# Kernel tuning notes

Hardware: AMD Instinct MI355X
Metric: run time of the kernel (lower is better)

Reference implementation:

```python
import jax, jax.numpy as jnp
import numpy as np

N = 100_000   # nodes
E = 1_600_000 # edges
F = 128       # node feature dim
H = 128       # hidden dim
A = 8         # num actions


def setup_inputs() -> dict:
    key = jax.random.key(0)
    ks = jax.random.split(key, 8)
    x = jax.random.normal(ks[0], (N, F), dtype=jnp.float32)
    edge_index = jax.random.randint(ks[1], (2, E), 0, N, dtype=jnp.int64)
    s1 = 1.0 / np.sqrt(F)
    s2 = 1.0 / np.sqrt(H)
    W1 = jax.random.uniform(ks[2], (F, H), jnp.float32, -s1, s1)
    b1 = jnp.zeros((H,), jnp.float32)
    W2 = jax.random.uniform(ks[3], (H, H), jnp.float32, -s2, s2)
    b2 = jnp.zeros((H,), jnp.float32)
    Wfc = jax.random.uniform(ks[4], (H, A), jnp.float32, -s2, s2)
    bfc = jax.random.uniform(ks[5], (A,), jnp.float32, -s2, s2)
    return {"x": x, "edge_index": edge_index, "W1": W1, "b1": b1,
            "W2": W2, "b2": b2, "Wfc": Wfc, "bfc": bfc}


def _gcn_norm(edge_index):
    # PyG GCNConv default: add self-loops, symmetric deg^{-1/2} A deg^{-1/2}
    src, dst = edge_index[0], edge_index[1]
    loop = jnp.arange(N, dtype=src.dtype)
    src_f = jnp.concatenate([src, loop])
    dst_f = jnp.concatenate([dst, loop])
    deg = jax.ops.segment_sum(jnp.ones((E + N,), jnp.float32), dst_f,
                              num_segments=N)
    dis = jax.lax.rsqrt(deg)  # deg >= 1 thanks to self-loops
    norm = dis[src_f] * dis[dst_f]  # [E+N]
    return src_f, dst_f, norm


def _gcn_conv(h, W, b, src_f, dst_f, norm):
    hw = h @ W                              # [N, out]
    msg = hw[src_f] * norm[:, None]         # gather + scale: [E+N, out]
    out = jax.ops.segment_sum(msg, dst_f, num_segments=N)  # scatter-add
    return out + b


def reference(x, edge_index, W1, b1, W2, b2, Wfc, bfc):
    src_f, dst_f, norm = _gcn_norm(edge_index)
    h = jax.nn.relu(_gcn_conv(x, W1, b1, src_f, dst_f, norm))
    h = jax.nn.relu(_gcn_conv(h, W2, b2, src_f, dst_f, norm))
    return h @ Wfc + bfc  # [N, A] per-node Q-values
```

## Files before the change

kernel.cpp:

```cpp
#include <hip/hip_runtime.h>
#include <hip/hip_bf16.h>

#define NN 100000
#define EE 1600000
#define FF 128
#define HH 128
#define AA 8

#define NBIN 782
#define CAP  3072

typedef unsigned int u32;
typedef unsigned short ushort_t;

using bf16x8 = __attribute__((ext_vector_type(8))) short;
using f32x4  = __attribute__((ext_vector_type(4))) float;

__device__ inline u32 packbf2(float a, float b) {
    __hip_bfloat162 t;
    t.x = __float2bfloat16(a);
    t.y = __float2bfloat16(b);
    return *(u32*)&t;
}
__device__ inline float2 unpackbf2(u32 v) {
    union { u32 u; float f; } lo, hi;
    lo.u = v << 16;
    hi.u = v & 0xffff0000u;
    return make_float2(lo.f, hi.f);
}

__global__ void k_init(int* bincnt) {
    int i = blockIdx.x * blockDim.x + threadIdx.x;
    if (i < NBIN) bincnt[i] = 0;
}

__global__ __launch_bounds__(256)
void k_wt(const float* __restrict__ W, u32* __restrict__ WT) {
    __shared__ float tile[32][33];
    const int tk = (blockIdx.x >> 2) * 32;
    const int tn = (blockIdx.x & 3) * 32;
    const int t = threadIdx.x;
    {
        int r = t >> 3, c4 = t & 7;
        float4 v = *(const float4*)&W[(tk + r) * 128 + tn + c4 * 4];
        tile[r][c4 * 4 + 0] = v.x;
        tile[r][c4 * 4 + 1] = v.y;
        tile[r][c4 * 4 + 2] = v.z;
        tile[r][c4 * 4 + 3] = v.w;
    }
    __syncthreads();
    {
        int nl = t >> 3, w = t & 7;
        u32 w0 = packbf2(tile[w * 4 + 0][nl], tile[w * 4 + 1][nl]);
        u32 w1 = packbf2(tile[w * 4 + 2][nl], tile[w * 4 + 3][nl]);
        *(uint2*)&WT[(size_t)(tn + nl) * 64 + (tk >> 1) + w * 2] = make_uint2(w0, w1);
    }
}

__global__ __launch_bounds__(256)
void k_bin(const int* __restrict__ ei, int* __restrict__ g_bincnt,
           int2* __restrict__ binbuf, int e) {
    __shared__ int cnt_l[NBIN];
    __shared__ int base_l[NBIN];
    __shared__ int cur_l[NBIN];
    const int t = threadIdx.x;
    for (int q = t; q < NBIN; q += 256) cnt_l[q] = 0;
    __syncthreads();
    const int per = (e + gridDim.x - 1) / gridDim.x;
    const int i0 = blockIdx.x * per;
    const int i1 = min(e, i0 + per);
    for (int i = i0 + t; i < i1; i += 256) {
        int dst = ei[e + i];
        atomicAdd(&cnt_l[dst >> 7], 1);
    }
    __syncthreads();
    for (int q = t; q < NBIN; q += 256) {
        base_l[q] = cnt_l[q] ? atomicAdd(&g_bincnt[q], cnt_l[q]) : 0;
        cur_l[q] = 0;
    }
    __syncthreads();
    for (int i = i0 + t; i < i1; i += 256) {
        int dst = ei[e + i];
        int src = ei[i];
        int p = dst >> 7;
        int pos = base_l[p] + atomicAdd(&cur_l[p], 1);
        if (pos < CAP)
            binbuf[(size_t)p * CAP + pos] = make_int2(src, dst);
    }
}

__global__ __launch_bounds__(1024)
void k_binscan(const int* __restrict__ bincnt, int* __restrict__ binbase) {
    __shared__ int s[1024];
    const int t = threadIdx.x;
    int v = (t < NBIN) ? min(bincnt[t], CAP) : 0;
    s[t] = v;
    __syncthreads();
    for (int off = 1; off < 1024; off <<= 1) {
        int x = (t >= off) ? s[t - off] : 0;
        __syncthreads();
        s[t] += x;
        __syncthreads();
    }
    if (t < NBIN) binbase[t] = s[t] - v;
}

__global__ __launch_bounds__(256)
void k_csr(const int2* __restrict__ binbuf, const int* __restrict__ g_bincnt,
           const int* __restrict__ binbase, int* __restrict__ row_start,
           float* __restrict__ dis, int* __restrict__ csr_src, int n)
{
    __shared__ int deg[128], s[128], cur[128];
    const int p = blockIdx.x;
    const int t = threadIdx.x;
    const int plo = p << 7;
    if (t < 128) { deg[t] = 0; cur[t] = 0; }
    __syncthreads();
    const int c = min(g_bincnt[p], CAP);
    const int2* slab = &binbuf[(size_t)p * CAP];
    for (int i = t; i < c; i += 256)
        atomicAdd(&deg[slab[i].y - plo], 1);
    __syncthreads();
    if (t < 128) s[t] = deg[t];
    __syncthreads();
    for (int off = 1; off < 128; off <<= 1) {
        int x = (t < 128 && t >= off) ? s[t - off] : 0;
        __syncthreads();
        if (t < 128) s[t] += x;
        __syncthreads();
    }
    const int base = binbase[p];
    if (t < 128) {
        int node = plo + t;
        if (node <= n) row_start[node] = base + s[t] - deg[t];
        if (node < n)  dis[node] = rsqrtf((float)deg[t] + 1.0f);
        if (p == NBIN - 1 && t == 127) row_start[n] = base + s[127];
    }
    __syncthreads();
    for (int i = t; i < c; i += 256) {
        int2 sd = slab[i];
        int nl = sd.y - plo;
        int pos = base + (s[nl] - deg[nl]) + atomicAdd(&cur[nl], 1);
        csr_src[pos] = sd.x;
    }
}

#define LDK 136

template<int AF32>
__global__ __launch_bounds__(256)
void k_gemm_mfma(const void* __restrict__ Ain, const u32* __restrict__ WT,
                 const float* __restrict__ dis, u32* __restrict__ outbf, int n)
{
    __shared__ ushort_t sA[64 * LDK];
    __shared__ ushort_t sB[128 * LDK];
    const int tid = threadIdx.x;
    const int row0 = blockIdx.x * 64;

    if (AF32) {
        const float* A = (const float*)Ain;
#pragma unroll
        for (int i = 0; i < 8; i++) {
            int f = tid + i * 256;
            int r = f >> 5, c4 = f & 31;
            int gr = row0 + r; if (gr >= n) gr = n - 1;
            float4 v = *(const float4*)&A[(size_t)gr * 128 + c4 * 4];
            *(uint2*)&sA[r * LDK + c4 * 4] =
                make_uint2(packbf2(v.x, v.y), packbf2(v.z, v.w));
        }
    } else {
        const u32* A = (const u32*)Ain;
#pragma unroll
        for (int i = 0; i < 4; i++) {
            int f = tid + i * 256;
            int r = f >> 4, q = f & 15;
            int gr = row0 + r; if (gr >= n) gr = n - 1;
            uint4 v = *(const uint4*)&A[(size_t)gr * 64 + q * 4];
            *(uint4*)&sA[r * LDK + q * 8] = v;
        }
    }
#pragma unroll
    for (int i = 0; i < 8; i++) {
        int f = tid + i * 256;
        int r = f >> 4, q = f & 15;
        uint4 v = *(const uint4*)&WT[(size_t)r * 64 + q * 4];
        *(uint4*)&sB[r * LDK + q * 8] = v;
    }
    __syncthreads();

    const int l   = tid & 63;
    const int w   = tid >> 6;
    const int col = l & 15;
    const int g   = l >> 4;
    const ushort_t* pa = &sA[(w * 16 + col) * LDK + g * 8];
    const ushort_t* pb = &sB[col * LDK + g * 8];

    f32x4 acc[8] = {};
#pragma unroll
    for (int ks = 0; ks < 4; ks++) {
        bf16x8 a = *(const bf16x8*)(pa + ks * 32);
#pragma unroll
        for (int cf = 0; cf < 8; cf++) {
            bf16x8 b = *(const bf16x8*)(pb + (size_t)cf * 16 * LDK + ks * 32);
            acc[cf] = __builtin_amdgcn_mfma_f32_16x16x32_bf16(a, b, acc[cf], 0, 0, 0);
        }
    }

    const int grow0 = row0 + w * 16 + g * 4;
    float dvr[4];
#pragma unroll
    for (int r = 0; r < 4; r++)
        dvr[r] = (grow0 + r < n) ? dis[grow0 + r] : 0.f;
#pragma unroll
    for (int cf = 0; cf < 8; cf++) {
#pragma unroll
        for (int r = 0; r < 4; r++) {
            float val = acc[cf][r] * dvr[r];
            float oth = __shfl_xor(val, 1);
            if (!(l & 1) && (grow0 + r < n))
                outbf[(size_t)(grow0 + r) * 64 + (cf * 16 + col) / 2] = packbf2(val, oth);
        }
    }
}

__launch_bounds__(256)
__global__ void k_agg(const int* __restrict__ csr_src,
                      const int* __restrict__ row_start,
                      const u32* __restrict__ hw,
                      const float* __restrict__ dis,
                      const float* __restrict__ b,
                      u32* __restrict__ out, int n)
{
    int node = blockIdx.x * 4 + (threadIdx.x >> 6);
    if (node >= n) return;
    int lane = threadIdx.x & 63;
    int beg = row_start[node];
    int end = row_start[node + 1];

    float2 acc = unpackbf2(hw[(long long)node * 64 + lane]);
    int i = beg;
    for (; i + 15 < end; i += 16) {
        int idx[16];
#pragma unroll
        for (int u = 0; u < 16; u++) idx[u] = csr_src[i + u];
        u32 a[16];
#pragma unroll
        for (int u = 0; u < 16; u++) a[u] = hw[(long long)idx[u] * 64 + lane];
        float sx = 0.f, sy = 0.f;
#pragma unroll
        for (int u = 0; u < 16; u++) {
            float2 v = unpackbf2(a[u]);
            sx += v.x; sy += v.y;
        }
        acc.x += sx; acc.y += sy;
    }
    if (i + 7 < end) {
        int idx[8];
#pragma unroll
        for (int u = 0; u < 8; u++) idx[u] = csr_src[i + u];
        u32 a[8];
#pragma unroll
        for (int u = 0; u < 8; u++) a[u] = hw[(long long)idx[u] * 64 + lane];
        float sx = 0.f, sy = 0.f;
#pragma unroll
        for (int u = 0; u < 8; u++) {
            float2 v = unpackbf2(a[u]);
            sx += v.x; sy += v.y;
        }
        acc.x += sx; acc.y += sy;
        i += 8;
    }
    for (; i + 1 < end; i += 2) {
        int s0 = csr_src[i];
        int s1 = csr_src[i + 1];
        float2 v0 = unpackbf2(hw[(long long)s0 * 64 + lane]);
        float2 v1 = unpackbf2(hw[(long long)s1 * 64 + lane]);
        acc.x += v0.x + v1.x;
        acc.y += v0.y + v1.y;
    }
    if (i < end) {
        float2 v0 = unpackbf2(hw[(long long)csr_src[i] * 64 + lane]);
        acc.x += v0.x;
        acc.y += v0.y;
    }
    float d = dis[node];
    float2 bb = *(const float2*)&b[lane * 2];
    float ox = fmaxf(fmaf(d, acc.x, bb.x), 0.f);
    float oy = fmaxf(fmaf(d, acc.y, bb.y), 0.f);
    out[(long long)node * 64 + lane] = packbf2(ox, oy);
}

__launch_bounds__(256)
__global__ void k_fc(const u32* __restrict__ hbf,
                     const float* __restrict__ Wfc,
                     const float* __restrict__ bfc,
                     float* __restrict__ out, int n)
{
    __shared__ float sW[128 * 8];
    __shared__ float sH[32][132];
    const int tid = threadIdx.x;
    *(float4*)&sW[tid * 4] = *(const float4*)&Wfc[tid * 4];
    const int n0 = blockIdx.x * 32;
#pragma unroll
    for (int i = 0; i < 4; i++) {
        int f = tid + i * 256;
        int node = f >> 5;
        int wq = f & 31;
        int gn = n0 + node; if (gn >= n) gn = n - 1;
        uint2 v = *(const uint2*)&hbf[(long long)gn * 64 + wq * 2];
        float2 p0 = unpackbf2(v.x);
        float2 p1 = unpackbf2(v.y);
        sH[node][wq * 4 + 0] = p0.x;
        sH[node][wq * 4 + 1] = p0.y;
        sH[node][wq * 4 + 2] = p1.x;
        sH[node][wq * 4 + 3] = p1.y;
    }
    __syncthreads();
    const int node = tid >> 3;
    const int a = tid & 7;
    float acc = bfc[a];
#pragma unroll
    for (int k = 0; k < 128; k++)
        acc += sH[node][k] * sW[k * 8 + a];
    int gn = n0 + node;
    if (gn < n) out[gn * 8 + a] = acc;
}

extern "C" void kernel_launch(void* const* d_in, const int* in_sizes, int n_in,
                              void* d_out, int out_size, void* d_ws, size_t ws_size,
                              hipStream_t stream) {
    const float* x   = (const float*)d_in[0];
    const int*   ei  = (const int*)d_in[1];
    const float* W1  = (const float*)d_in[2];
    const float* b1  = (const float*)d_in[3];
    const float* W2  = (const float*)d_in[4];
    const float* b2  = (const float*)d_in[5];
    const float* Wfc = (const float*)d_in[6];
    const float* bfc = (const float*)d_in[7];
    float* out = (float*)d_out;

    const int n = NN, e = EE;

    char* ws = (char*)d_ws;
    const size_t MB = 1 << 20;
    float* dis       = (float*)(ws);
    int*   row_start = (int*)  (ws + 512 * 1024);
    int*   bincnt    = (int*)  (ws + 1 * MB);
    int*   binbase   = (int*)  (ws + 1 * MB + 8192);
    u32*   WT1       = (u32*)  (ws + 1 * MB + 65536);
    u32*   WT2       = (u32*)  (ws + 1 * MB + 2 * 65536);
    int2*  binbuf    = (int2*) (ws + 2 * MB);
    int*   csr_src   = (int*)  (ws + 22 * MB);
    u32*   hwbf      = (u32*)  (ws + 29 * MB);
    u32*   hbf       = (u32*)  (ws + 55 * MB);

    k_init<<<(NBIN + 255) / 256, 256, 0, stream>>>(bincnt);
    k_wt<<<16, 256, 0, stream>>>(W1, WT1);
    k_wt<<<16, 256, 0, stream>>>(W2, WT2);

    k_bin<<<128, 256, 0, stream>>>(ei, bincnt, binbuf, e);
    k_binscan<<<1, 1024, 0, stream>>>(bincnt, binbase);
    k_csr<<<NBIN, 256, 0, stream>>>(binbuf, bincnt, binbase, row_start, dis, csr_src, n);

    const int gemm_grid = (n + 63) / 64;
    const int agg_grid  = (n + 3) / 4;

    k_gemm_mfma<1><<<gemm_grid, 256, 0, stream>>>(x, WT1, dis, hwbf, n);
    k_agg<<<agg_grid, 256, 0, stream>>>(csr_src, row_start, hwbf, dis, b1, hbf, n);

    k_gemm_mfma<0><<<gemm_grid, 256, 0, stream>>>(hbf, WT2, dis, hwbf, n);
    k_agg<<<agg_grid, 256, 0, stream>>>(csr_src, row_start, hwbf, dis, b2, hbf, n);

    k_fc<<<(n + 31) / 32, 256, 0, stream>>>(hbf, Wfc, bfc, out, n);
}
```

Before: 247.5 us.

## Vectorize edge binning loads and split wave halves across edges in aggregation

The binning kernel now runs 256 blocks of 1024 threads, and each thread reads int4 groups of edge indices, which cuts load instruction count and spreads the work over more CUs. The aggregation kernel has each half-wave take alternate edges, with every lane loading 8 bytes (4 bf16 features) instead of 4. The two halves are then combined with a cross-half shuffle before the bias, ReLU and store. This doubles the gathers in flight per wave and widens each memory access, at the cost of the shuffle reduction and half the lanes idling in the epilogue.

```diff
diff --git a/kernel.cpp b/kernel.cpp
--- a/kernel.cpp
+++ b/kernel.cpp
@@ -9,6 +9,7 @@
 
 #define NBIN 782
 #define CAP  3072
+#define BINBLK 256
 
 typedef unsigned int u32;
 typedef unsigned short ushort_t;
@@ -57,35 +58,53 @@
     }
 }
 
-__global__ __launch_bounds__(256)
+__global__ __launch_bounds__(1024)
 void k_bin(const int* __restrict__ ei, int* __restrict__ g_bincnt,
            int2* __restrict__ binbuf, int e) {
     __shared__ int cnt_l[NBIN];
     __shared__ int base_l[NBIN];
     __shared__ int cur_l[NBIN];
     const int t = threadIdx.x;
-    for (int q = t; q < NBIN; q += 256) cnt_l[q] = 0;
-    __syncthreads();
-    const int per = (e + gridDim.x - 1) / gridDim.x;
+    for (int q = t; q < NBIN; q += 1024) cnt_l[q] = 0;
+    __syncthreads();
+    const int per = (((e + BINBLK - 1) / BINBLK) + 3) & ~3;
     const int i0 = blockIdx.x * per;
     const int i1 = min(e, i0 + per);
-    for (int i = i0 + t; i < i1; i += 256) {
-        int dst = ei[e + i];
-        atomicAdd(&cnt_l[dst >> 7], 1);
-    }
-    __syncthreads();
-    for (int q = t; q < NBIN; q += 256) {
+    int i = i0 + t * 4;
+    for (; i + 3 < i1; i += 4096) {
+        int4 d4 = *(const int4*)&ei[e + i];
+        atomicAdd(&cnt_l[d4.x >> 7], 1);
+        atomicAdd(&cnt_l[d4.y >> 7], 1);
+        atomicAdd(&cnt_l[d4.z >> 7], 1);
+        atomicAdd(&cnt_l[d4.w >> 7], 1);
+    }
+    for (int j = i; j < min(i + 4, i1); j++)
+        atomicAdd(&cnt_l[ei[e + j] >> 7], 1);
+    __syncthreads();
+    for (int q = t; q < NBIN; q += 1024) {
         base_l[q] = cnt_l[q] ? atomicAdd(&g_bincnt[q], cnt_l[q]) : 0;
         cur_l[q] = 0;
     }
     __syncthreads();
-    for (int i = i0 + t; i < i1; i += 256) {
-        int dst = ei[e + i];
-        int src = ei[i];
+    i = i0 + t * 4;
+    for (; i + 3 < i1; i += 4096) {
+        int4 s4 = *(const int4*)&ei[i];
+        int4 d4 = *(const int4*)&ei[e + i];
+        int p0 = d4.x >> 7, p1 = d4.y >> 7, p2 = d4.z >> 7, p3 = d4.w >> 7;
+        int q0 = base_l[p0] + atomicAdd(&cur_l[p0], 1);
+        int q1 = base_l[p1] + atomicAdd(&cur_l[p1], 1);
+        int q2 = base_l[p2] + atomicAdd(&cur_l[p2], 1);
+        int q3 = base_l[p3] + atomicAdd(&cur_l[p3], 1);
+        if (q0 < CAP) binbuf[(size_t)p0 * CAP + q0] = make_int2(s4.x, d4.x);
+        if (q1 < CAP) binbuf[(size_t)p1 * CAP + q1] = make_int2(s4.y, d4.y);
+        if (q2 < CAP) binbuf[(size_t)p2 * CAP + q2] = make_int2(s4.z, d4.z);
+        if (q3 < CAP) binbuf[(size_t)p3 * CAP + q3] = make_int2(s4.w, d4.w);
+    }
+    for (int j = i; j < min(i + 4, i1); j++) {
+        int dst = ei[e + j], src = ei[j];
         int p = dst >> 7;
         int pos = base_l[p] + atomicAdd(&cur_l[p], 1);
-        if (pos < CAP)
-            binbuf[(size_t)p * CAP + pos] = make_int2(src, dst);
+        if (pos < CAP) binbuf[(size_t)p * CAP + pos] = make_int2(src, dst);
     }
 }
 
@@ -233,61 +252,58 @@
 {
     int node = blockIdx.x * 4 + (threadIdx.x >> 6);
     if (node >= n) return;
-    int lane = threadIdx.x & 63;
-    int beg = row_start[node];
-    int end = row_start[node + 1];
-
-    float2 acc = unpackbf2(hw[(long long)node * 64 + lane]);
+    const int lane = threadIdx.x & 63;
+    const int half = lane >> 5;
+    const int sl   = lane & 31;
+    const int beg = row_start[node];
+    const int end = row_start[node + 1];
+
+    float4 acc = make_float4(0.f, 0.f, 0.f, 0.f);
+    if (!half) {
+        uint2 s = *(const uint2*)&hw[(size_t)node * 64 + sl * 2];
+        float2 a = unpackbf2(s.x), c = unpackbf2(s.y);
+        acc = make_float4(a.x, a.y, c.x, c.y);
+    }
     int i = beg;
     for (; i + 15 < end; i += 16) {
-        int idx[16];
-#pragma unroll
-        for (int u = 0; u < 16; u++) idx[u] = csr_src[i + u];
-        u32 a[16];
-#pragma unroll
-        for (int u = 0; u < 16; u++) a[u] = hw[(long long)idx[u] * 64 + lane];
-        float sx = 0.f, sy = 0.f;
-#pragma unroll
-        for (int u = 0; u < 16; u++) {
-            float2 v = unpackbf2(a[u]);
-            sx += v.x; sy += v.y;
-        }
-        acc.x += sx; acc.y += sy;
-    }
-    if (i + 7 < end) {
         int idx[8];
 #pragma unroll
-        for (int u = 0; u < 8; u++) idx[u] = csr_src[i + u];
-        u32 a[8];
-#pragma unroll
-        for (int u = 0; u < 8; u++) a[u] = hw[(long long)idx[u] * 64 + lane];
-        float sx = 0.f, sy = 0.f;
+        for (int u = 0; u < 8; u++) idx[u] = csr_src[i + 2 * u + half];
+        uint2 v[8];
+#pragma unroll
+        for (int u = 0; u < 8; u++) v[u] = *(const uint2*)&hw[(size_t)idx[u] * 64 + sl * 2];
 #pragma unroll
         for (int u = 0; u < 8; u++) {
-            float2 v = unpackbf2(a[u]);
-            sx += v.x; sy += v.y;
-        }
-        acc.x += sx; acc.y += sy;
-        i += 8;
+            float2 a = unpackbf2(v[u].x), c = unpackbf2(v[u].y);
+            acc.x += a.x; acc.y += a.y; acc.z += c.x; acc.w += c.y;
+        }
     }
     for (; i + 1 < end; i += 2) {
-        int s0 = csr_src[i];
-        int s1 = csr_src[i + 1];
-        float2 v0 = unpackbf2(hw[(long long)s0 * 64 + lane]);
-        float2 v1 = unpackbf2(hw[(long long)s1 * 64 + lane]);
-        acc.x += v0.x + v1.x;
-        acc.y += v0.y + v1.y;
-    }
-    if (i < end) {
-        float2 v0 = unpackbf2(hw[(long long)csr_src[i] * 64 + lane]);
-        acc.x += v0.x;
-        acc.y += v0.y;
-    }
-    float d = dis[node];
-    float2 bb = *(const float2*)&b[lane * 2];
-    float ox = fmaxf(fmaf(d, acc.x, bb.x), 0.f);
-    float oy = fmaxf(fmaf(d, acc.y, bb.y), 0.f);
-    out[(long long)node * 64 + lane] = packbf2(ox, oy);
+        int idx = csr_src[i + half];
+        uint2 v = *(const uint2*)&hw[(size_t)idx * 64 + sl * 2];
+        float2 a = unpackbf2(v.x), c = unpackbf2(v.y);
+        acc.x += a.x; acc.y += a.y; acc.z += c.x; acc.w += c.y;
+    }
+    if (i < end && !half) {
+        uint2 v = *(const uint2*)&hw[(size_t)csr_src[i] * 64 + sl * 2];
+        float2 a = unpackbf2(v.x), c = unpackbf2(v.y);
+        acc.x += a.x; acc.y += a.y; acc.z += c.x; acc.w += c.y;
+    }
+    acc.x += __shfl_xor(acc.x, 32);
+    acc.y += __shfl_xor(acc.y, 32);
+    acc.z += __shfl_xor(acc.z, 32);
+    acc.w += __shfl_xor(acc.w, 32);
+
+    if (!half) {
+        float d = dis[node];
+        float4 bb = *(const float4*)&b[sl * 4];
+        float ox = fmaxf(fmaf(d, acc.x, bb.x), 0.f);
+        float oy = fmaxf(fmaf(d, acc.y, bb.y), 0.f);
+        float oz = fmaxf(fmaf(d, acc.z, bb.z), 0.f);
+        float ow = fmaxf(fmaf(d, acc.w, bb.w), 0.f);
+        *(uint2*)&out[(size_t)node * 64 + sl * 2] =
+            make_uint2(packbf2(ox, oy), packbf2(oz, ow));
+    }
 }
 
 __launch_bounds__(256)
@@ -358,7 +374,7 @@
     k_wt<<<16, 256, 0, stream>>>(W1, WT1);
     k_wt<<<16, 256, 0, stream>>>(W2, WT2);
 
-    k_bin<<<128, 256, 0, stream>>>(ei, bincnt, binbuf, e);
+    k_bin<<<BINBLK, 1024, 0, stream>>>(ei, bincnt, binbuf, e);
     k_binscan<<<1, 1024, 0, stream>>>(bincnt, binbase);
     k_csr<<<NBIN, 256, 0, stream>>>(binbuf, bincnt, binbase, row_start, dis, csr_src, n);
 
```

Result: no change. 242.6 us (-2.0%).
